# Performance work log

Measured on AMD Instinct MI355X. Metric: run time of the kernel, lower is better.

Reference implementation:

```python
import jax, jax.numpy as jnp
import numpy as np

B, T, C, H = 8, 1024, 768, 12
HD = C // H
EPS = 1e-5
NEG = jnp.finfo(jnp.float32).min


def layer_norm(x, scale, bias):
    mu = jnp.mean(x, axis=-1, keepdims=True)
    var = jnp.mean(jnp.square(x - mu), axis=-1, keepdims=True)
    return (x - mu) * jax.lax.rsqrt(var + EPS) * scale + bias


def setup_inputs() -> dict:
    key = jax.random.key(0)
    ks = jax.random.split(key, 8)
    s = lambda fan_in: 1.0 / np.sqrt(fan_in)
    x = jax.random.normal(ks[0], (B, T, C), dtype=jnp.float32)
    mask = jnp.tril(jnp.ones((T, T), dtype=bool))[None, None, :, :]
    return {
        "x": x,
        "mask": mask,
        "ln1_scale": jnp.ones((C,), jnp.float32),
        "ln1_bias": jnp.zeros((C,), jnp.float32),
        "w_qkv": jax.random.normal(ks[1], (C, 3 * C), jnp.float32) * s(C),
        "b_qkv": jnp.zeros((3 * C,), jnp.float32),
        "w_attn_proj": jax.random.normal(ks[2], (C, C), jnp.float32) * s(C),
        "b_attn_proj": jnp.zeros((C,), jnp.float32),
        "ln2_scale": jnp.ones((C,), jnp.float32),
        "ln2_bias": jnp.zeros((C,), jnp.float32),
        "w_fc": jax.random.normal(ks[3], (C, 4 * C), jnp.float32) * s(C),
        "b_fc": jnp.zeros((4 * C,), jnp.float32),
        "w_mlp_proj": jax.random.normal(ks[4], (4 * C, C), jnp.float32) * s(4 * C),
        "b_mlp_proj": jnp.zeros((C,), jnp.float32),
    }


def reference(x, mask, ln1_scale, ln1_bias, w_qkv, b_qkv, w_attn_proj,
              b_attn_proj, ln2_scale, ln2_bias, w_fc, b_fc, w_mlp_proj,
              b_mlp_proj):
    # --- attention branch (pre-LN) ---
    h = layer_norm(x, ln1_scale, ln1_bias)
    qkv = jnp.einsum('btc,cd->btd', h, w_qkv) + b_qkv      # [B,T,3C]
    qkv = qkv.reshape(B, T, 3 * H, HD)
    q, k, v = jnp.array_split(qkv, 3, axis=2)              # each [B,T,H,HD]
    scale = 1.0 / jnp.sqrt(jnp.float32(HD))
    attn = jnp.einsum('bqhd,bkhd->bhqk', q, k) * scale     # [B,H,T,T]
    attn = jnp.where(mask, attn, NEG)
    attn = jax.nn.softmax(attn, axis=-1)
    ctx = jnp.einsum('bhqk,bkhd->bqhd', attn, v).reshape(B, T, C)
    attn_out = jnp.einsum('btc,cd->btd', ctx, w_attn_proj) + b_attn_proj
    x = x + attn_out
    # --- MLP branch (pre-LN) ---
    h = layer_norm(x, ln2_scale, ln2_bias)
    h = jax.nn.gelu(jnp.einsum('btc,cf->btf', h, w_fc) + b_fc)  # tanh approx, as flax default
    mlp_out = jnp.einsum('btf,fc->btc', h, w_mlp_proj) + b_mlp_proj
    return x + mlp_out
```

## Files before the change

### kernel.cpp

```cpp
#include <hip/hip_runtime.h>
#include <hip/hip_bf16.h>
#include <cstdint>
#include <math.h>

#define BB 8
#define TT 1024
#define CC 768
#define HH 12
#define MROWS (BB*TT)

typedef __hip_bfloat16 bf16;
typedef __attribute__((ext_vector_type(8))) __bf16 bf16x8;
typedef __attribute__((ext_vector_type(4))) float f32x4;

#define MFMA16(a,b,c) __builtin_amdgcn_mfma_f32_16x16x32_bf16(a,b,c,0,0,0)

__device__ __forceinline__ void gload_lds16(const bf16* g, bf16* l) {
  __builtin_amdgcn_global_load_lds(
      (__attribute__((address_space(1))) void*)(g),
      (__attribute__((address_space(3))) void*)(l), 16, 0, 0);
}

__global__ __launch_bounds__(256) void ln_kernel(
    const float* __restrict__ x, const float* __restrict__ scale,
    const float* __restrict__ bias, bf16* __restrict__ out)
{
  int row = blockIdx.x;
  const float* xr = x + (size_t)row * CC;
  float v[3];
  float s = 0.f, s2 = 0.f;
  for (int i = 0; i < 3; i++) {
    v[i] = xr[threadIdx.x + i*256];
    s += v[i]; s2 += v[i]*v[i];
  }
  for (int m = 1; m < 64; m <<= 1) { s += __shfl_xor(s, m); s2 += __shfl_xor(s2, m); }
  __shared__ float ssum[4], ssum2[4];
  int w = threadIdx.x >> 6;
  if ((threadIdx.x & 63) == 0) { ssum[w] = s; ssum2[w] = s2; }
  __syncthreads();
  s = ssum[0]+ssum[1]+ssum[2]+ssum[3];
  s2 = ssum2[0]+ssum2[1]+ssum2[2]+ssum2[3];
  float mu = s * (1.f/CC);
  float var = s2 * (1.f/CC) - mu*mu;
  float rs = rsqrtf(var + 1e-5f);
  bf16* orow = out + (size_t)row * CC;
  for (int i = 0; i < 3; i++) {
    int c = threadIdx.x + i*256;
    orow[c] = __float2bfloat16((v[i]-mu)*rs*scale[c] + bias[c]);
  }
}

__global__ __launch_bounds__(256) void wtrans_kernel(
    const float* __restrict__ src, bf16* __restrict__ dst, int K, int N)
{
  __shared__ float tile[32][33];
  int n0 = blockIdx.x * 32, k0 = blockIdx.y * 32;
  int tx = threadIdx.x & 31, ty = threadIdx.x >> 5;
  for (int i = 0; i < 4; i++)
    tile[ty + i*8][tx] = src[(size_t)(k0 + ty + i*8)*N + n0 + tx];
  __syncthreads();
  for (int i = 0; i < 4; i++)
    dst[(size_t)(n0 + ty + i*8)*K + k0 + tx] = __float2bfloat16(tile[tx][ty + i*8]);
}

__global__ __launch_bounds__(256) void vtrans_kernel(
    const bf16* __restrict__ src, bf16* __restrict__ dst)
{
  __shared__ bf16 tile[64][65];
  int bh = blockIdx.x >> 4, t0 = (blockIdx.x & 15) * 64;
  const bf16* s = src + ((size_t)bh * TT + t0) * 64;
  for (int i = 0; i < 16; i++) {
    int idx = threadIdx.x + i*256;
    tile[idx >> 6][idx & 63] = s[idx];
  }
  __syncthreads();
  bf16* o = dst + (size_t)bh * 64 * TT + t0;
  for (int i = 0; i < 16; i++) {
    int idx = threadIdx.x + i*256;
    int d = idx >> 6, t = idx & 63;
    o[(size_t)d * TT + t] = tile[t][d];
  }
}

template<int EPI>
__global__ __launch_bounds__(256) void gemm_bt(
    const bf16* __restrict__ A, const bf16* __restrict__ Bt,
    const float* __restrict__ bias, int Mdim, int Ndim, int Kdim,
    const float* __restrict__ res, void* __restrict__ out0,
    bf16* __restrict__ outK, bf16* __restrict__ outV)
{
  __shared__ bf16 As[2][128*32];
  __shared__ bf16 Bs[2][128*32];
  int tid = threadIdx.x;
  int wave = tid >> 6, lane = tid & 63;
  int quad = lane >> 4, l15 = lane & 15;
  int wr = wave >> 1, wc = wave & 1;

  int Nb = gridDim.x;
  int lin = blockIdx.y * Nb + blockIdx.x;
  int band = lin / (8*Nb);
  int rem  = lin - band*8*Nb;
  int m0 = (band*8 + (rem & 7)) * 128;
  int n0 = (rem >> 3) * 128;

  const int sub = lane >> 2;
  const int kk = (lane & 3) * 8;

  f32x4 acc[4][4];
  for (int i = 0; i < 4; i++) for (int j = 0; j < 4; j++)
    acc[i][j] = (f32x4){0.f,0.f,0.f,0.f};

  const int niter = Kdim >> 5;
  for (int q = 0; q < 2; q++) {
    int seg = q*4 + wave;
    gload_lds16(A + (size_t)(m0 + seg*16 + sub) * Kdim + kk, As[0] + seg*512 + lane*8);
    gload_lds16(Bt + (size_t)(n0 + seg*16 + sub) * Kdim + kk, Bs[0] + seg*512 + lane*8);
  }

  for (int it = 0; it < niter; it++) {
    int cur = it & 1, nxt = cur ^ 1;
    __syncthreads();
    if (it + 1 < niter) {
      int kt = (it + 1) << 5;
      for (int q = 0; q < 2; q++) {
        int seg = q*4 + wave;
        gload_lds16(A + (size_t)(m0 + seg*16 + sub) * Kdim + kt + kk,
                    As[nxt] + seg*512 + lane*8);
        gload_lds16(Bt + (size_t)(n0 + seg*16 + sub) * Kdim + kt + kk,
                    Bs[nxt] + seg*512 + lane*8);
      }
    }
    bf16x8 af[4], bfr[4];
    for (int i = 0; i < 4; i++)
      af[i] = *reinterpret_cast<const bf16x8*>(As[cur] + (wr*64 + i*16 + l15)*32 + quad*8);
    for (int j = 0; j < 4; j++)
      bfr[j] = *reinterpret_cast<const bf16x8*>(Bs[cur] + (wc*64 + j*16 + l15)*32 + quad*8);
    for (int i = 0; i < 4; i++)
      for (int j = 0; j < 4; j++)
        acc[i][j] = MFMA16(af[i], bfr[j], acc[i][j]);
  }

  for (int i = 0; i < 4; i++) {
    for (int j = 0; j < 4; j++) {
      for (int r = 0; r < 4; r++) {
        int row = m0 + wr*64 + i*16 + quad*4 + r;
        int col = n0 + wc*64 + j*16 + l15;
        float cv = acc[i][j][r] + bias[col];
        if (EPI == 0) {
          int part = col / 768;
          int cc = col - part*768;
          int h = cc >> 6, d = cc & 63;
          int b = row >> 10, t = row & 1023;
          bf16* dst = (part == 0) ? (bf16*)out0 : (part == 1) ? outK : outV;
          dst[(((size_t)(b*HH + h))*TT + t)*64 + d] = __float2bfloat16(cv);
        } else if (EPI == 1) {
          ((float*)out0)[(size_t)row*Ndim + col] = cv + res[(size_t)row*Ndim + col];
        } else {
          float u = cv;
          float y = 0.7978845608f*(u + 0.044715f*u*u*u);
          float e = __expf(2.f*fabsf(y));
          float z = 2.f/(e + 1.f);
          float sel = (y >= 0.f) ? (2.f - z) : z;
          ((bf16*)out0)[(size_t)row*Ndim + col] = __float2bfloat16(0.5f*u*sel);
        }
      }
    }
  }
}

__global__ __launch_bounds__(256) void attn_kernel(
    const bf16* __restrict__ Q, const bf16* __restrict__ Kb,
    const bf16* __restrict__ Vt, bf16* __restrict__ ctx)
{
  __shared__ bf16 Ks[64*64];
  __shared__ bf16 Vs[64*64];
  __shared__ bf16 Ps[4*16*64];

  int tid = threadIdx.x, wave = tid >> 6, lane = tid & 63;
  int quad = lane >> 4, l15 = lane & 15;
  int bh = blockIdx.x >> 4;
  int tile = 15 - (blockIdx.x & 15);
  int q0b = tile*64;
  int q0w = q0b + wave*16;
  int b = bh / HH, h = bh - b*HH;
  const bf16* Qp = Q + ((size_t)bh*TT + q0w)*64;
  const bf16* Kp = Kb + (size_t)bh*TT*64;
  const bf16* Vp = Vt + (size_t)bh*64*TT;
  bf16* Pw = Ps + wave*16*64;

  bf16x8 qf[2];
  qf[0] = *reinterpret_cast<const bf16x8*>(Qp + l15*64 + quad*8);
  qf[1] = *reinterpret_cast<const bf16x8*>(Qp + l15*64 + 32 + quad*8);

  f32x4 O[4];
  for (int j = 0; j < 4; j++) O[j] = (f32x4){0.f,0.f,0.f,0.f};
  float lsum[4] = {0.f, 0.f, 0.f, 0.f};
  const float c2 = 0.18033688f;

  const int srow0 = wave*16 + (lane >> 3);
  const int sc    = lane & 7;

  int nc = tile + 1;

  bf16x8 kreg[2], vreg[2], kreg2[2], vreg2[2];
  for (int rep = 0; rep < 2; rep++) {
    int row = srow0 + rep*8;
    kreg[rep] = *reinterpret_cast<const bf16x8*>(Kp + (size_t)row*64 + sc*8);
    vreg[rep] = *reinterpret_cast<const bf16x8*>(Vp + (size_t)row*TT + sc*8);
  }

  for (int ci = 0; ci < nc; ci++) {
    int kbase = ci*64;
    __syncthreads();
    for (int rep = 0; rep < 2; rep++) {
      int row = srow0 + rep*8;
      int ph = sc ^ (row & 7);
      *reinterpret_cast<bf16x8*>(Ks + row*64 + ph*8) = kreg[rep];
      *reinterpret_cast<bf16x8*>(Vs + row*64 + ph*8) = vreg[rep];
    }
    if (ci + 1 < nc) {
      int kb2 = kbase + 64;
      for (int rep = 0; rep < 2; rep++) {
        int row = srow0 + rep*8;
        kreg2[rep] = *reinterpret_cast<const bf16x8*>(Kp + (size_t)(kb2 + row)*64 + sc*8);
        vreg2[rep] = *reinterpret_cast<const bf16x8*>(Vp + (size_t)row*TT + kb2 + sc*8);
      }
    }
    __syncthreads();

    f32x4 S[4];
    for (int j = 0; j < 4; j++) S[j] = (f32x4){0.f,0.f,0.f,0.f};
    for (int kh = 0; kh < 2; kh++) {
      for (int j = 0; j < 4; j++) {
        int key = j*16 + l15;
        bf16x8 kf = *reinterpret_cast<const bf16x8*>(
            Ks + key*64 + ((kh*4 + quad) ^ (key & 7))*8);
        S[j] = MFMA16(qf[kh], kf, S[j]);
      }
    }

    float p[4][4];
    if (kbase + 63 > q0w) {
      for (int j = 0; j < 4; j++) {
        int key = kbase + j*16 + l15;
        for (int r = 0; r < 4; r++) {
          int row = q0w + quad*4 + r;
          p[j][r] = (key <= row) ? __builtin_amdgcn_exp2f(S[j][r]*c2) : 0.f;
        }
      }
    } else {
      for (int j = 0; j < 4; j++)
        for (int r = 0; r < 4; r++)
          p[j][r] = __builtin_amdgcn_exp2f(S[j][r]*c2);
    }
    for (int j = 0; j < 4; j++)
      for (int r = 0; r < 4; r++) lsum[r] += p[j][r];

    for (int j = 0; j < 4; j++) {
      int cblk = j*2 + (l15 >> 3);
      int koff = l15 & 7;
      for (int r = 0; r < 4; r++) {
        int q = quad*4 + r;
        Pw[q*64 + (cblk ^ (q & 7))*8 + koff] = __float2bfloat16(p[j][r]);
      }
    }

    for (int kh = 0; kh < 2; kh++) {
      bf16x8 pf = *reinterpret_cast<const bf16x8*>(
          Pw + l15*64 + ((kh*4 + quad) ^ (l15 & 7))*8);
      for (int j = 0; j < 4; j++) {
        int d = j*16 + l15;
        bf16x8 vf = *reinterpret_cast<const bf16x8*>(
            Vs + d*64 + ((kh*4 + quad) ^ (d & 7))*8);
        O[j] = MFMA16(pf, vf, O[j]);
      }
    }

    for (int rep = 0; rep < 2; rep++) { kreg[rep] = kreg2[rep]; vreg[rep] = vreg2[rep]; }
  }

  for (int r = 0; r < 4; r++)
    for (int msk = 1; msk < 16; msk <<= 1)
      lsum[r] += __shfl_xor(lsum[r], msk);

  bf16* cp = ctx + ((size_t)b*TT + q0w)*CC + h*64;
  for (int r = 0; r < 4; r++) {
    float inv = 1.f / lsum[r];
    int row = quad*4 + r;
    for (int j = 0; j < 4; j++)
      cp[(size_t)row*CC + j*16 + l15] = __float2bfloat16(O[j][r]*inv);
  }
}

extern "C" void kernel_launch(void* const* d_in, const int* in_sizes, int n_in,
                              void* d_out, int out_size, void* d_ws, size_t ws_size,
                              hipStream_t stream)
{
  const float* x    = (const float*)d_in[0];
  const float* ln1s = (const float*)d_in[2];
  const float* ln1b = (const float*)d_in[3];
  const float* wqkv = (const float*)d_in[4];
  const float* bqkv = (const float*)d_in[5];
  const float* wap  = (const float*)d_in[6];
  const float* bap  = (const float*)d_in[7];
  const float* ln2s = (const float*)d_in[8];
  const float* ln2b = (const float*)d_in[9];
  const float* wfc  = (const float*)d_in[10];
  const float* bfc  = (const float*)d_in[11];
  const float* wmp  = (const float*)d_in[12];
  const float* bmp  = (const float*)d_in[13];

  char* ws = (char*)d_ws;
  bf16* wqkv_t = (bf16*)ws; ws += (size_t)2304*768*2;
  bf16* wap_t  = (bf16*)ws; ws += (size_t)768*768*2;
  bf16* wfc_t  = (bf16*)ws; ws += (size_t)3072*768*2;
  bf16* wmp_t  = (bf16*)ws; ws += (size_t)768*3072*2;
  bf16* buf1   = (bf16*)ws; ws += (size_t)MROWS*CC*2;
  bf16* Qb     = (bf16*)ws; ws += (size_t)MROWS*CC*2;
  bf16* Kbuf   = (bf16*)ws; ws += (size_t)MROWS*CC*2;
  bf16* Vb     = (bf16*)ws; ws += (size_t)MROWS*CC*2;
  bf16* Vt     = (bf16*)ws; ws += (size_t)MROWS*CC*2;
  bf16* g      = Qb;
  float* r1    = (float*)ws; ws += (size_t)MROWS*CC*4;

  dim3 blk(256);
  wtrans_kernel<<<dim3(2304/32, 768/32), blk, 0, stream>>>(wqkv, wqkv_t, 768, 2304);
  wtrans_kernel<<<dim3(768/32, 768/32), blk, 0, stream>>>(wap, wap_t, 768, 768);
  wtrans_kernel<<<dim3(3072/32, 768/32), blk, 0, stream>>>(wfc, wfc_t, 768, 3072);
  wtrans_kernel<<<dim3(768/32, 3072/32), blk, 0, stream>>>(wmp, wmp_t, 3072, 768);
  ln_kernel<<<MROWS, blk, 0, stream>>>(x, ln1s, ln1b, buf1);
  gemm_bt<0><<<dim3(2304/128, MROWS/128), blk, 0, stream>>>(
      buf1, wqkv_t, bqkv, MROWS, 2304, 768, nullptr, (void*)Qb, Kbuf, Vb);
  vtrans_kernel<<<BB*HH*16, blk, 0, stream>>>(Vb, Vt);
  attn_kernel<<<BB*HH*16, blk, 0, stream>>>(Qb, Kbuf, Vt, buf1);
  gemm_bt<1><<<dim3(768/128, MROWS/128), blk, 0, stream>>>(
      buf1, wap_t, bap, MROWS, 768, 768, x, (void*)r1, nullptr, nullptr);
  ln_kernel<<<MROWS, blk, 0, stream>>>(r1, ln2s, ln2b, buf1);
  gemm_bt<2><<<dim3(3072/128, MROWS/128), blk, 0, stream>>>(
      buf1, wfc_t, bfc, MROWS, 3072, 768, nullptr, (void*)g, nullptr, nullptr);
  gemm_bt<1><<<dim3(768/128, MROWS/128), blk, 0, stream>>>(
      g, wmp_t, bmp, MROWS, 768, 3072, r1, d_out, nullptr, nullptr);
}
```

Baseline: 398.5 us.

## Stage GEMM tiles through registers instead of direct global-to-LDS loads

Replaces the global_load_lds direct-to-LDS prefetch in the GEMM main loop with register-staged prefetch. Next-tile global loads are issued into registers before the MFMAs and written to the other LDS buffer afterwards, followed by a lightweight waitcnt plus s_barrier instead of __syncthreads. A-fragment loads are also interleaved with the MFMAs. The aim is to hide global latency behind compute and cut barrier overhead, at the cost of extra VGPRs and explicit LDS stores.

```diff
diff --git a/kernel.cpp b/kernel.cpp
--- a/kernel.cpp
+++ b/kernel.cpp
@@ -15,10 +15,8 @@
 
 #define MFMA16(a,b,c) __builtin_amdgcn_mfma_f32_16x16x32_bf16(a,b,c,0,0,0)
 
-__device__ __forceinline__ void gload_lds16(const bf16* g, bf16* l) {
-  __builtin_amdgcn_global_load_lds(
-      (__attribute__((address_space(1))) void*)(g),
-      (__attribute__((address_space(3))) void*)(l), 16, 0, 0);
+__device__ __forceinline__ void lds_barrier() {
+  asm volatile("s_waitcnt lgkmcnt(0)\n\ts_barrier" ::: "memory");
 }
 
 __global__ __launch_bounds__(256) void ln_kernel(
@@ -110,34 +108,51 @@
   for (int i = 0; i < 4; i++) for (int j = 0; j < 4; j++)
     acc[i][j] = (f32x4){0.f,0.f,0.f,0.f};
 
+  const bf16* pa0 = A  + (size_t)(m0 + wave*16      + sub)*Kdim + kk;
+  const bf16* pa1 = A  + (size_t)(m0 + (4+wave)*16  + sub)*Kdim + kk;
+  const bf16* pb0 = Bt + (size_t)(n0 + wave*16      + sub)*Kdim + kk;
+  const bf16* pb1 = Bt + (size_t)(n0 + (4+wave)*16  + sub)*Kdim + kk;
+  const int woff0 = wave*512     + lane*8;
+  const int woff1 = (4+wave)*512 + lane*8;
+
   const int niter = Kdim >> 5;
-  for (int q = 0; q < 2; q++) {
-    int seg = q*4 + wave;
-    gload_lds16(A + (size_t)(m0 + seg*16 + sub) * Kdim + kk, As[0] + seg*512 + lane*8);
-    gload_lds16(Bt + (size_t)(n0 + seg*16 + sub) * Kdim + kk, Bs[0] + seg*512 + lane*8);
-  }
+
+  bf16x8 ra0 = *reinterpret_cast<const bf16x8*>(pa0);
+  bf16x8 ra1 = *reinterpret_cast<const bf16x8*>(pa1);
+  bf16x8 rb0 = *reinterpret_cast<const bf16x8*>(pb0);
+  bf16x8 rb1 = *reinterpret_cast<const bf16x8*>(pb1);
+  pa0 += 32; pa1 += 32; pb0 += 32; pb1 += 32;
+  *reinterpret_cast<bf16x8*>(As[0] + woff0) = ra0;
+  *reinterpret_cast<bf16x8*>(As[0] + woff1) = ra1;
+  *reinterpret_cast<bf16x8*>(Bs[0] + woff0) = rb0;
+  *reinterpret_cast<bf16x8*>(Bs[0] + woff1) = rb1;
+  lds_barrier();
 
   for (int it = 0; it < niter; it++) {
     int cur = it & 1, nxt = cur ^ 1;
-    __syncthreads();
-    if (it + 1 < niter) {
-      int kt = (it + 1) << 5;
-      for (int q = 0; q < 2; q++) {
-        int seg = q*4 + wave;
-        gload_lds16(A + (size_t)(m0 + seg*16 + sub) * Kdim + kt + kk,
-                    As[nxt] + seg*512 + lane*8);
-        gload_lds16(Bt + (size_t)(n0 + seg*16 + sub) * Kdim + kt + kk,
-                    Bs[nxt] + seg*512 + lane*8);
-      }
-    }
-    bf16x8 af[4], bfr[4];
-    for (int i = 0; i < 4; i++)
-      af[i] = *reinterpret_cast<const bf16x8*>(As[cur] + (wr*64 + i*16 + l15)*32 + quad*8);
+    bool more = (it + 1 < niter);
+    if (more) {
+      ra0 = *reinterpret_cast<const bf16x8*>(pa0);
+      ra1 = *reinterpret_cast<const bf16x8*>(pa1);
+      rb0 = *reinterpret_cast<const bf16x8*>(pb0);
+      rb1 = *reinterpret_cast<const bf16x8*>(pb1);
+      pa0 += 32; pa1 += 32; pb0 += 32; pb1 += 32;
+    }
+    bf16x8 bfr[4];
     for (int j = 0; j < 4; j++)
       bfr[j] = *reinterpret_cast<const bf16x8*>(Bs[cur] + (wc*64 + j*16 + l15)*32 + quad*8);
-    for (int i = 0; i < 4; i++)
+    for (int i = 0; i < 4; i++) {
+      bf16x8 af = *reinterpret_cast<const bf16x8*>(As[cur] + (wr*64 + i*16 + l15)*32 + quad*8);
       for (int j = 0; j < 4; j++)
-        acc[i][j] = MFMA16(af[i], bfr[j], acc[i][j]);
+        acc[i][j] = MFMA16(af, bfr[j], acc[i][j]);
+    }
+    if (more) {
+      *reinterpret_cast<bf16x8*>(As[nxt] + woff0) = ra0;
+      *reinterpret_cast<bf16x8*>(As[nxt] + woff1) = ra1;
+      *reinterpret_cast<bf16x8*>(Bs[nxt] + woff0) = rb0;
+      *reinterpret_cast<bf16x8*>(Bs[nxt] + woff1) = rb1;
+      lds_barrier();
+    }
   }
 
   for (int i = 0; i < 4; i++) {
```

New measurement: 375.4 us. -5.8%, faster.
